# Optimization experiments

Hardware: AMD Instinct MI355X
Metric: run time of the kernel (lower is better)

The kernel has to match this reference:

```python
import jax, jax.numpy as jnp
from jax import lax
import numpy as np

C_IN = 64
C_OUT = 64
CQ = C_OUT // 8   # query/key channels
K = 5             # axial kernel length
RATIO = 0.7       # hybrid-norm mixing ratio
EPS = 1e-5
DN = ('NCHW', 'OIHW', 'NCHW')


def setup_inputs() -> dict:
    key = jax.random.key(0)
    ks = jax.random.split(key, 16)
    rn = lambda k, s, sc=0.05: jax.random.normal(k, s, dtype=jnp.float32) * sc
    return dict(
        x=jax.random.normal(ks[0], (4, C_IN, 256, 256), dtype=jnp.float32),
        hconv_w=rn(ks[1], (C_IN, 1, 1, K)), hconv_b=rn(ks[2], (C_IN,)),
        vconv_w=rn(ks[3], (C_IN, 1, K, 1)), vconv_b=rn(ks[4], (C_IN,)),
        pw_w=rn(ks[5], (C_OUT, C_IN)), pw_b=rn(ks[6], (C_OUT,)),
        bn_w=1.0 + rn(ks[7], (C_OUT,)), bn_b=rn(ks[8], (C_OUT,)),
        q_w=rn(ks[9], (CQ, C_OUT)), q_b=rn(ks[10], (CQ,)),
        k_w=rn(ks[11], (CQ, C_OUT)), k_b=rn(ks[12], (CQ,)),
        v_w=rn(ks[13], (C_OUT, C_OUT)), v_b=rn(ks[14], (C_OUT,)),
        gamma=rn(ks[15], (1,), 0.1),
    )


def reference(x, hconv_w, hconv_b, vconv_w, vconv_b, pw_w, pw_b,
              bn_w, bn_b, q_w, q_b, k_w, k_b, v_w, v_b, gamma):
    # ---- AxialDepthwiseConv: depthwise (1,K) + (K,1) + x, relu, pointwise ----
    h = lax.conv_general_dilated(x, hconv_w, (1, 1), [(0, 0), (K // 2, K // 2)],
                                 dimension_numbers=DN, feature_group_count=C_IN)
    h = h + hconv_b[:, None, None]
    v = lax.conv_general_dilated(x, vconv_w, (1, 1), [(K // 2, K // 2), (0, 0)],
                                 dimension_numbers=DN, feature_group_count=C_IN)
    v = v + vconv_b[:, None, None]
    a = jax.nn.relu(h + v + x)
    y = jnp.einsum('bchw,oc->bohw', a, pw_w) + pw_b[:, None, None]

    # ---- HybridNormalization: 0.7*InstanceNorm(no affine) + 0.3*BatchNorm(train) ----
    im = y.mean((2, 3), keepdims=True)
    iv = y.var((2, 3), keepdims=True)
    inn = (y - im) * lax.rsqrt(iv + EPS)
    bm = y.mean((0, 2, 3), keepdims=True)
    bv = y.var((0, 2, 3), keepdims=True)
    bnn = (y - bm) * lax.rsqrt(bv + EPS) * bn_w[:, None, None] + bn_b[:, None, None]
    y = RATIO * inn + (1.0 - RATIO) * bnn

    # ---- CrissCrossAttention ----
    q = jnp.einsum('bchw,oc->bohw', y, q_w) + q_b[:, None, None]   # (B,CQ,H,W)
    k = jnp.einsum('bchw,oc->bohw', y, k_w) + k_b[:, None, None]   # (B,CQ,H,W)
    val = jnp.einsum('bchw,oc->bohw', y, v_w) + v_b[:, None, None] # (B,C,H,W)

    # height (per column w): attn[b,w,j,i] = softmax_i( q[b,:,j,w] . k[b,:,i,w] )
    Ah = jax.nn.softmax(jnp.einsum('bcjw,bciw->bwji', q, k), axis=-1)
    # h_out[b,c,i,w] = sum_j val[b,c,j,w] * Ah[b,w,j,i]  (matches bmm(value, attn))
    h_out = jnp.einsum('bcjw,bwji->bciw', val, Ah)

    # width (per row h): attn[b,h,y,x] = softmax_x( q[b,:,h,y] . k[b,:,h,x] )
    Av = jax.nn.softmax(jnp.einsum('bchy,bchx->bhyx', q, k), axis=-1)
    v_out = jnp.einsum('bchy,bhyx->bchx', val, Av)

    out = gamma[0] * (h_out + v_out) + y

    # ---- MaxPool2d(2,2) ----
    down = lax.reduce_window(out, -jnp.inf, lax.max, (1, 1, 2, 2), (1, 1, 2, 2), 'VALID')
    return out, down
```

## Files before the change

kernel.cpp:

```cpp
#include <hip/hip_runtime.h>
#include <hip/hip_bf16.h>

#define Bn 4
#define Cc 64
#define CQn 8
#define Hh 256
#define Ww 256
#define PLANE 65536
#define LOG2E 1.4426950408889634f

typedef unsigned short ushortT;
typedef __attribute__((ext_vector_type(8))) unsigned short us8;
typedef __attribute__((ext_vector_type(4))) unsigned short us4;
typedef __attribute__((ext_vector_type(8))) __bf16 bf16x8;
typedef __attribute__((ext_vector_type(4))) float f32x4;

__device__ inline ushortT f2bf(float f) {
    __hip_bfloat16 h = __float2bfloat16(f);
    return *(ushortT*)&h;
}
__device__ inline float bf2f(ushortT u) {
    return __uint_as_float((unsigned)u << 16);
}
union BF8U { us8 u; bf16x8 b; uint4 w; };
__device__ inline us8 zero_us8() {
    BF8U z; z.w.x = 0; z.w.y = 0; z.w.z = 0; z.w.w = 0; return z.u;
}

__global__ void pack_weights_kernel(
    const float* __restrict__ pww, const float* __restrict__ qw,
    const float* __restrict__ kw, const float* __restrict__ vw,
    ushortT* __restrict__ pw_bf, ushortT* __restrict__ qk_bf,
    ushortT* __restrict__ vw_bf)
{
    int i = blockIdx.x * 256 + threadIdx.x;
    if (i < 64 * 64) pw_bf[i] = f2bf(pww[i]);
    if (i < 64 * 64) vw_bf[i] = f2bf(vw[i]);
    if (i < 8 * 64)  qk_bf[i] = f2bf(qw[i]);
    if (i >= 8 * 64 && i < 16 * 64) qk_bf[i] = f2bf(kw[i - 512]);
}

__global__ __launch_bounds__(256) void dw_kernel(
    const float* __restrict__ x,
    const float* __restrict__ hw, const float* __restrict__ hb,
    const float* __restrict__ vw, const float* __restrict__ vb,
    ushortT* __restrict__ aout)
{
    int blk = blockIdx.x;
    int bc = blk >> 4;
    int ht = blk & 15;
    int h0 = ht * 16;
    int c = bc & 63;
    int tid = threadIdx.x;
    __shared__ float rows[20][260];
    const float* xp = x + (size_t)bc * PLANE;
    #pragma unroll
    for (int i = 0; i < 20; ++i) {
        int hr = h0 - 2 + i;
        rows[i][tid + 2] = (hr >= 0 && hr < Hh) ? xp[hr * Ww + tid] : 0.f;
    }
    if (tid < 20) {
        rows[tid][0] = 0.f; rows[tid][1] = 0.f;
        rows[tid][258] = 0.f; rows[tid][259] = 0.f;
    }
    __syncthreads();

    float hw0 = hw[c * 5 + 0], hw1 = hw[c * 5 + 1], hw2 = hw[c * 5 + 2],
          hw3 = hw[c * 5 + 3], hw4 = hw[c * 5 + 4];
    float vw0 = vw[c * 5 + 0], vw1 = vw[c * 5 + 1], vw2 = vw[c * 5 + 2],
          vw3 = vw[c * 5 + 3], vw4 = vw[c * 5 + 4];
    float bias = hb[c] + vb[c];

    ushortT* op = aout + (size_t)bc * PLANE + h0 * Ww + tid;
    #pragma unroll
    for (int r = 0; r < 16; ++r) {
        float hs = hw0 * rows[r + 2][tid]     + hw1 * rows[r + 2][tid + 1]
                 + hw2 * rows[r + 2][tid + 2] + hw3 * rows[r + 2][tid + 3]
                 + hw4 * rows[r + 2][tid + 4];
        float vs = vw0 * rows[r][tid + 2]     + vw1 * rows[r + 1][tid + 2]
                 + vw2 * rows[r + 2][tid + 2] + vw3 * rows[r + 3][tid + 2]
                 + vw4 * rows[r + 4][tid + 2];
        float res = hs + vs + bias + rows[r + 2][tid + 2];
        op[r * Ww] = f2bf(fmaxf(res, 0.f));
    }
}

__global__ __launch_bounds__(256) void pw_mfma_kernel(
    const ushortT* __restrict__ a_bf, const ushortT* __restrict__ pw_bf,
    const float* __restrict__ pwb,
    float* __restrict__ y_raw, float* __restrict__ sums, float* __restrict__ sumsq)
{
    int blk = blockIdx.x;
    int b = blk >> 8;
    int t0 = (blk & 255) << 8;
    int tid = threadIdx.x, lane = tid & 63, wv = tid >> 6;
    int half = lane >> 4;
    int col = lane & 15;

    __shared__ ushortT ytile[256 * 74];

    {
        size_t base = (size_t)b * Cc * PLANE + t0 + tid;
        uint* wrow = (uint*)&ytile[tid * 74];
        #pragma unroll
        for (int c = 0; c < Cc; c += 2) {
            ushortT v0 = a_bf[base + (size_t)c * PLANE];
            ushortT v1 = a_bf[base + (size_t)(c + 1) * PLANE];
            wrow[c >> 1] = (uint)v0 | ((uint)v1 << 16);
        }
    }
    __syncthreads();

    int m0 = wv * 16;
    BF8U a0, a1;
    a0.u = *(const us8*)(pw_bf + (m0 + col) * 64 + half * 8);
    a1.u = *(const us8*)(pw_bf + (m0 + col) * 64 + 32 + half * 8);

    float bias[4], s[4], s2[4];
    #pragma unroll
    for (int r = 0; r < 4; ++r) {
        bias[r] = pwb[m0 + half * 4 + r];
        s[r] = 0.f; s2[r] = 0.f;
    }

    const uint* lw = (const uint*)ytile;
    #pragma unroll 4
    for (int t = 0; t < 16; ++t) {
        int rbase = (t * 16 + col) * 37 + half * 4;
        BF8U b0, b1;
        b0.w.x = lw[rbase];      b0.w.y = lw[rbase + 1];
        b0.w.z = lw[rbase + 2];  b0.w.w = lw[rbase + 3];
        b1.w.x = lw[rbase + 16]; b1.w.y = lw[rbase + 17];
        b1.w.z = lw[rbase + 18]; b1.w.w = lw[rbase + 19];
        f32x4 acc = (f32x4){0.f, 0.f, 0.f, 0.f};
        acc = __builtin_amdgcn_mfma_f32_16x16x32_bf16(a0.b, b0.b, acc, 0, 0, 0);
        acc = __builtin_amdgcn_mfma_f32_16x16x32_bf16(a1.b, b1.b, acc, 0, 0, 0);
        int pix = t * 16 + col;
        #pragma unroll
        for (int r = 0; r < 4; ++r) {
            int c = m0 + half * 4 + r;
            float v = acc[r] + bias[r];
            y_raw[(size_t)(b * Cc + c) * PLANE + t0 + pix] = v;
            s[r] += v; s2[r] += v * v;
        }
    }
    #pragma unroll
    for (int r = 0; r < 4; ++r) {
        #pragma unroll
        for (int d = 8; d > 0; d >>= 1) {
            s[r]  += __shfl_down(s[r], d, 16);
            s2[r] += __shfl_down(s2[r], d, 16);
        }
    }
    if (col == 0) {
        #pragma unroll
        for (int r = 0; r < 4; ++r) {
            int c = m0 + half * 4 + r;
            atomicAdd(&sums[b * Cc + c], s[r]);
            atomicAdd(&sumsq[b * Cc + c], s2[r]);
        }
    }
}

__global__ __launch_bounds__(256) void qkv_mfma_kernel(
    const float* __restrict__ y_raw,
    const float* __restrict__ sums, const float* __restrict__ sumsq,
    const float* __restrict__ bnw, const float* __restrict__ bnb,
    const ushortT* __restrict__ qk_bf, const float* __restrict__ qbias,
    const float* __restrict__ kbias,
    const ushortT* __restrict__ vw_bf, const float* __restrict__ vbias,
    ushortT* __restrict__ q, ushortT* __restrict__ k,
    ushortT* __restrict__ val)
{
    int blk = blockIdx.x;
    int b = blk >> 8;
    int t0 = (blk & 255) << 8;
    int tid = threadIdx.x, lane = tid & 63, wv = tid >> 6;
    int half = lane >> 4;
    int col = lane & 15;

    __shared__ ushortT ytile[256 * 74];
    __shared__ float alpha_s[64], beta_s[64];

    if (tid < 64) {
        int c = tid;
        float im[4], e2[4];
        float bm = 0.f, be2 = 0.f;
        #pragma unroll
        for (int bb = 0; bb < 4; ++bb) {
            im[bb] = sums[bb * Cc + c] * (1.f / 65536.f);
            e2[bb] = sumsq[bb * Cc + c] * (1.f / 65536.f);
            bm += im[bb]; be2 += e2[bb];
        }
        bm *= 0.25f; be2 *= 0.25f;
        float rsb = rsqrtf(be2 - bm * bm + 1e-5f);
        float wgt = bnw[c];
        float rsi = rsqrtf(e2[b] - im[b] * im[b] + 1e-5f);
        alpha_s[c] = 0.7f * rsi + 0.3f * rsb * wgt;
        beta_s[c]  = -0.7f * im[b] * rsi - 0.3f * bm * rsb * wgt + 0.3f * bnb[c];
    }
    __syncthreads();

    {
        size_t base = (size_t)b * Cc * PLANE + t0 + tid;
        uint* wrow = (uint*)&ytile[tid * 74];
        #pragma unroll
        for (int c = 0; c < Cc; c += 2) {
            float v0 = y_raw[base + (size_t)c * PLANE];
            float v1 = y_raw[base + (size_t)(c + 1) * PLANE];
            float n0 = alpha_s[c] * v0 + beta_s[c];
            float n1 = alpha_s[c + 1] * v1 + beta_s[c + 1];
            wrow[c >> 1] = (uint)f2bf(n0) | ((uint)f2bf(n1) << 16);
        }
    }
    __syncthreads();

    const uint* lw = (const uint*)ytile;

    {
        BF8U a0, a1;
        a0.u = *(const us8*)(qk_bf + col * 64 + half * 8);
        a1.u = *(const us8*)(qk_bf + col * 64 + 32 + half * 8);
        #pragma unroll
        for (int i = 0; i < 4; ++i) {
            int t = wv * 4 + i;
            int rbase = (t * 16 + col) * 37 + half * 4;
            BF8U b0, b1;
            b0.w.x = lw[rbase];      b0.w.y = lw[rbase + 1];
            b0.w.z = lw[rbase + 2];  b0.w.w = lw[rbase + 3];
            b1.w.x = lw[rbase + 16]; b1.w.y = lw[rbase + 17];
            b1.w.z = lw[rbase + 18]; b1.w.w = lw[rbase + 19];
            f32x4 acc = (f32x4){0.f, 0.f, 0.f, 0.f};
            acc = __builtin_amdgcn_mfma_f32_16x16x32_bf16(a0.b, b0.b, acc, 0, 0, 0);
            acc = __builtin_amdgcn_mfma_f32_16x16x32_bf16(a1.b, b1.b, acc, 0, 0, 0);
            int pix = t * 16 + col;
            #pragma unroll
            for (int r = 0; r < 4; ++r) {
                int row = half * 4 + r;
                if (row < 8)
                    q[(size_t)(b * CQn + row) * PLANE + t0 + pix] =
                        f2bf((acc[r] + qbias[row]) * LOG2E);
                else
                    k[(size_t)(b * CQn + row - 8) * PLANE + t0 + pix] = f2bf(acc[r] + kbias[row - 8]);
            }
        }
    }

    {
        int m0 = wv * 16;
        BF8U a0, a1;
        a0.u = *(const us8*)(vw_bf + (m0 + col) * 64 + half * 8);
        a1.u = *(const us8*)(vw_bf + (m0 + col) * 64 + 32 + half * 8);
        float bias[4];
        #pragma unroll
        for (int r = 0; r < 4; ++r) bias[r] = vbias[m0 + half * 4 + r];
        #pragma unroll 4
        for (int t = 0; t < 16; ++t) {
            int rbase = (t * 16 + col) * 37 + half * 4;
            BF8U b0, b1;
            b0.w.x = lw[rbase];      b0.w.y = lw[rbase + 1];
            b0.w.z = lw[rbase + 2];  b0.w.w = lw[rbase + 3];
            b1.w.x = lw[rbase + 16]; b1.w.y = lw[rbase + 17];
            b1.w.z = lw[rbase + 18]; b1.w.w = lw[rbase + 19];
            f32x4 acc = (f32x4){0.f, 0.f, 0.f, 0.f};
            acc = __builtin_amdgcn_mfma_f32_16x16x32_bf16(a0.b, b0.b, acc, 0, 0, 0);
            acc = __builtin_amdgcn_mfma_f32_16x16x32_bf16(a1.b, b1.b, acc, 0, 0, 0);
            int pix = t * 16 + col;
            #pragma unroll
            for (int r = 0; r < 4; ++r) {
                int c = m0 + half * 4 + r;
                val[(size_t)(b * Cc + c) * PLANE + t0 + pix] = f2bf(acc[r] + bias[r]);
            }
        }
    }
}

__global__ __launch_bounds__(256) void transpose_all_kernel(
    const ushortT* __restrict__ qb, ushortT* __restrict__ qT,
    const ushortT* __restrict__ kb, ushortT* __restrict__ kT,
    const ushortT* __restrict__ vb, ushortT* __restrict__ vT)
{
    int blk = blockIdx.x;
    int plane = blk >> 6;
    int tile = blk & 63;
    const ushortT* src; ushortT* dst;
    if (plane < 32)      { src = qb + (size_t)plane * PLANE;        dst = qT + (size_t)plane * PLANE; }
    else if (plane < 64) { src = kb + (size_t)(plane - 32) * PLANE; dst = kT + (size_t)(plane - 32) * PLANE; }
    else                 { src = vb + (size_t)(plane - 64) * PLANE; dst = vT + (size_t)(plane - 64) * PLANE; }
    int th = (tile >> 3) * 32;
    int tw = (tile & 7) * 32;
    __shared__ ushortT t[32][34];
    int lw = threadIdx.x & 31;
    int lh = threadIdx.x >> 5;
    #pragma unroll
    for (int i = 0; i < 4; ++i)
        t[lh + 8 * i][lw] = src[(th + lh + 8 * i) * Ww + tw + lw];
    __syncthreads();
    #pragma unroll
    for (int i = 0; i < 4; ++i)
        dst[(tw + lh + 8 * i) * Hh + th + lw] = t[lw][lh + 8 * i];
}

__global__ __launch_bounds__(256) void attn_kernel(
    const ushortT* __restrict__ q0, const ushortT* __restrict__ k0,
    const ushortT* __restrict__ v0, ushortT* __restrict__ o0,
    const ushortT* __restrict__ q1, const ushortT* __restrict__ k1,
    const ushortT* __restrict__ v1, ushortT* __restrict__ o1)
{
    int blk = blockIdx.x;
    int sel = blk >> 10;
    const ushortT* __restrict__ q   = sel ? q1 : q0;
    const ushortT* __restrict__ k   = sel ? k1 : k0;
    const ushortT* __restrict__ val = sel ? v1 : v0;
    ushortT* __restrict__ outp      = sel ? o1 : o0;
    int bblk = blk & 1023;
    int b = bblk >> 8;
    int r = bblk & 255;
    int tid = threadIdx.x;
    int lane = tid & 63;
    int wv = tid >> 6;
    int col = lane & 15;
    int quad = lane >> 4;

    __shared__ ushortT q_s[256 * 8];
    __shared__ ushortT k_s[256 * 8];
    __shared__ ushortT A_lds[2][4 * 256 * 8];
    __shared__ float mhat[256];
    __shared__ float kred[32];
    __shared__ float lsum[2][4][32];

    size_t vbase = (size_t)b * Cc * PLANE + (size_t)r * Ww
                 + (size_t)(wv * 16 + col) * PLANE + quad * 8;
    BF8U afb[2];
    afb[0].u = *(const us8*)(val + vbase);

    size_t qkbase = (size_t)b * CQn * PLANE + (size_t)r * Ww + tid;
    float qf[8], ka[8];
    {
        BF8U qp, kp;
        #pragma unroll
        for (int c = 0; c < 8; ++c) {
            ushortT qv = q[qkbase + (size_t)c * PLANE];
            ushortT kv = k[qkbase + (size_t)c * PLANE];
            qp.u[c] = qv; kp.u[c] = kv;
            qf[c] = bf2f(qv);
            ka[c] = fabsf(bf2f(kv));
        }
        *(us8*)&q_s[tid * 8] = qp.u;
        *(us8*)&k_s[tid * 8] = kp.u;
    }
    #pragma unroll
    for (int d = 1; d < 64; d <<= 1)
        #pragma unroll
        for (int c = 0; c < 8; ++c)
            ka[c] = fmaxf(ka[c], __shfl_xor(ka[c], d));
    if (lane == 0)
        #pragma unroll
        for (int c = 0; c < 8; ++c) kred[wv * 8 + c] = ka[c];
    __syncthreads();

    {
        float mh = 0.f;
        #pragma unroll
        for (int c = 0; c < 8; ++c) {
            float km = fmaxf(fmaxf(kred[c], kred[8 + c]),
                             fmaxf(kred[16 + c], kred[24 + c]));
            mh += fabsf(qf[c]) * km;
        }
        mhat[tid] = mh;
    }
    __syncthreads();

    BF8U kc[4];
    #pragma unroll
    for (int i = 0; i < 4; ++i)
        kc[i].u = *(const us8*)&k_s[((wv * 4 + i) * 16 + col) * 8];
    f32x4 acc[16];
    #pragma unroll
    for (int t = 0; t < 16; ++t) acc[t] = (f32x4){0.f, 0.f, 0.f, 0.f};

    auto compute_slab = [&](int kslab, int buf) {
        float ps[8];
        #pragma unroll
        for (int e = 0; e < 8; ++e) ps[e] = 0.f;
        #pragma unroll
        for (int jj2 = 0; jj2 < 2; ++jj2) {
            int jt = kslab * 2 + jj2;
            BF8U qa; qa.u = zero_us8();
            if (quad == 0) qa.u = *(const us8*)&q_s[(jt * 16 + col) * 8];
            float mh4[4];
            #pragma unroll
            for (int rr = 0; rr < 4; ++rr) mh4[rr] = mhat[jt * 16 + quad * 4 + rr];
            #pragma unroll
            for (int i = 0; i < 4; ++i) {
                f32x4 sacc = (f32x4){0.f, 0.f, 0.f, 0.f};
                sacc = __builtin_amdgcn_mfma_f32_16x16x32_bf16(qa.b, kc[i].b, sacc, 0, 0, 0);
                us4 pk;
                #pragma unroll
                for (int rr = 0; rr < 4; ++rr) {
                    float e = __builtin_amdgcn_exp2f(sacc[rr] - mh4[rr]);
                    ps[jj2 * 4 + rr] += e;
                    pk[rr] = f2bf(e);
                }
                int irow = (wv * 4 + i) * 16 + col;
                int jq = jj2 * 2 + (quad >> 1);
                *(us4*)&A_lds[buf][(jq * 256 + irow) * 8 + (quad & 1) * 4] = pk;
            }
        }
        #pragma unroll
        for (int d = 1; d < 16; d <<= 1)
            #pragma unroll
            for (int e = 0; e < 8; ++e)
                ps[e] += __shfl_xor(ps[e], d);
        if (col == 0) {
            #pragma unroll
            for (int jj2 = 0; jj2 < 2; ++jj2)
                #pragma unroll
                for (int rr = 0; rr < 4; ++rr)
                    lsum[buf][wv][jj2 * 16 + quad * 4 + rr] = ps[jj2 * 4 + rr];
        }
    };

    compute_slab(0, 0);
    __syncthreads();

    #pragma unroll
    for (int ks = 0; ks < 8; ++ks) {
        int cur = ks & 1;
        if (ks < 7) {
            afb[cur ^ 1].u = *(const us8*)(val + vbase + (ks + 1) * 32);
            compute_slab(ks + 1, cur ^ 1);
        }
        f32x4 l0 = *(const f32x4*)&lsum[cur][0][quad * 8];
        f32x4 l1 = *(const f32x4*)&lsum[cur][0][quad * 8 + 4];
        #pragma unroll
        for (int w = 1; w < 4; ++w) {
            l0 += *(const f32x4*)&lsum[cur][w][quad * 8];
            l1 += *(const f32x4*)&lsum[cur][w][quad * 8 + 4];
        }
        BF8U av;
        #pragma unroll
        for (int e = 0; e < 4; ++e) {
            av.u[e]     = f2bf(bf2f(afb[cur].u[e])     * __builtin_amdgcn_rcpf(l0[e]));
            av.u[4 + e] = f2bf(bf2f(afb[cur].u[4 + e]) * __builtin_amdgcn_rcpf(l1[e]));
        }
        #pragma unroll
        for (int t = 0; t < 16; ++t) {
            BF8U bfr;
            bfr.u = *(const us8*)&A_lds[cur][(quad * 256 + t * 16 + col) * 8];
            acc[t] = __builtin_amdgcn_mfma_f32_16x16x32_bf16(av.b, bfr.b, acc[t], 0, 0, 0);
        }
        __syncthreads();
    }

    size_t obase = (size_t)b * Cc * PLANE + (size_t)r * Ww;
    #pragma unroll
    for (int t = 0; t < 16; ++t) {
        int i = t * 16 + col;
        #pragma unroll
        for (int rr = 0; rr < 4; ++rr) {
            int c = wv * 16 + quad * 4 + rr;
            outp[obase + (size_t)c * PLANE + i] = f2bf(acc[t][rr]);
        }
    }
}

__global__ __launch_bounds__(256) void final_kernel(
    const ushortT* __restrict__ houtT, const ushortT* __restrict__ hout0,
    const float* __restrict__ y_raw,
    const float* __restrict__ sums, const float* __restrict__ sumsq,
    const float* __restrict__ bnw, const float* __restrict__ bnb,
    const float* __restrict__ gamma,
    float* __restrict__ out, float* __restrict__ down)
{
    int blk = blockIdx.x;
    int tile = blk & 63;
    int bc = blk >> 6;
    int b = bc >> 6;
    int c = bc & 63;
    int th = (tile >> 3) * 32;
    int tw = (tile & 7) * 32;

    float im[4], e2[4];
    float bm = 0.f, be2 = 0.f;
    #pragma unroll
    for (int bb = 0; bb < 4; ++bb) {
        im[bb] = sums[bb * Cc + c] * (1.f / 65536.f);
        e2[bb] = sumsq[bb * Cc + c] * (1.f / 65536.f);
        bm += im[bb]; be2 += e2[bb];
    }
    bm *= 0.25f; be2 *= 0.25f;
    float rsb = rsqrtf(be2 - bm * bm + 1e-5f);
    float wgt = bnw[c];
    float rsi = rsqrtf(e2[b] - im[b] * im[b] + 1e-5f);
    float al = 0.7f * rsi + 0.3f * rsb * wgt;
    float bt = -0.7f * im[b] * rsi - 0.3f * bm * rsb * wgt + 0.3f * bnb[c];

    __shared__ float t[32][33];
    const ushortT* hT = houtT + (size_t)bc * PLANE;
    {
        int ww = threadIdx.x >> 3;
        int hh = (threadIdx.x & 7) * 4;
        us4 v4 = *(const us4*)(hT + (size_t)(tw + ww) * Hh + th + hh);
        t[hh + 0][ww] = __uint_as_float((unsigned)v4[0] << 16);
        t[hh + 1][ww] = __uint_as_float((unsigned)v4[1] << 16);
        t[hh + 2][ww] = __uint_as_float((unsigned)v4[2] << 16);
        t[hh + 3][ww] = __uint_as_float((unsigned)v4[3] << 16);
    }
    __syncthreads();
    float g = gamma[0];
    int qw_ = threadIdx.x & 15;
    int qh_ = threadIdx.x >> 4;
    const float* yb = y_raw + (size_t)bc * PLANE;
    const ushortT* hb = hout0 + (size_t)bc * PLANE;
    float* ob = out + (size_t)bc * PLANE;
    float mx = -1e30f;
    float2 res[2];
    #pragma unroll
    for (int i = 0; i < 2; ++i) {
        int hh = 2 * qh_ + i;
        int off = (th + hh) * Ww + tw + 2 * qw_;
        uint hv = *(const uint*)(hb + off);
        float2 y = *(const float2*)(yb + off);
        float y0 = al * y.x + bt;
        float y1 = al * y.y + bt;
        float o0 = g * (t[hh][2 * qw_]     + bf2f((ushortT)(hv & 0xffff))) + y0;
        float o1 = g * (t[hh][2 * qw_ + 1] + bf2f((ushortT)(hv >> 16)))   + y1;
        res[i] = make_float2(o0, o1);
        mx = fmaxf(mx, fmaxf(o0, o1));
    }
    #pragma unroll
    for (int i = 0; i < 2; ++i) {
        int off = (th + 2 * qh_ + i) * Ww + tw + 2 * qw_;
        *(float2*)(ob + off) = res[i];
    }
    down[(size_t)bc * 16384 + (th / 2 + qh_) * 128 + tw / 2 + qw_] = mx;
}

extern "C" void kernel_launch(void* const* d_in, const int* in_sizes, int n_in,
                              void* d_out, int out_size, void* d_ws, size_t ws_size,
                              hipStream_t stream)
{
    const float* x     = (const float*)d_in[0];
    const float* hw    = (const float*)d_in[1];
    const float* hb    = (const float*)d_in[2];
    const float* vw    = (const float*)d_in[3];
    const float* vb    = (const float*)d_in[4];
    const float* pww   = (const float*)d_in[5];
    const float* pwb   = (const float*)d_in[6];
    const float* bnw   = (const float*)d_in[7];
    const float* bnb   = (const float*)d_in[8];
    const float* qw    = (const float*)d_in[9];
    const float* qb    = (const float*)d_in[10];
    const float* kw    = (const float*)d_in[11];
    const float* kb    = (const float*)d_in[12];
    const float* vw2   = (const float*)d_in[13];
    const float* vb2   = (const float*)d_in[14];
    const float* gamma = (const float*)d_in[15];

    float* ws = (float*)d_ws;
    const size_t NP = (size_t)Bn * Cc * PLANE;
    const size_t NQ = (size_t)Bn * CQn * PLANE;
    float* y_raw  = ws;
    float* slotB  = ws + NP;
    float* slotC  = ws + 2 * NP;
    float* slotD  = ws + 2 * NP + NP / 2;
    float* ptr    = ws + 3 * NP;
    ushortT* qbuf = (ushortT*)ptr;
    ushortT* kbuf = qbuf + NQ;
    ushortT* qT   = kbuf + NQ;
    ushortT* kT   = qT + NQ;
    float* sums   = (float*)(kT + NQ);
    float* sumsq  = sums + 256;
    ushortT* pw_bf = (ushortT*)(sumsq + 256);
    ushortT* qk_bf = pw_bf + 64 * 64;
    ushortT* vw_bf = qk_bf + 16 * 64;

    ushortT* a_buf = (ushortT*)slotC;
    ushortT* valT  = (ushortT*)slotC;
    ushortT* valb  = (ushortT*)slotD;
    ushortT* hout0 = (ushortT*)slotB;
    ushortT* houtT = hout0 + NP;
    float* out  = (float*)d_out;
    float* down = out + NP;

    hipMemsetAsync(sums, 0, 512 * sizeof(float), stream);
    pack_weights_kernel<<<dim3(16), dim3(256), 0, stream>>>(
        pww, qw, kw, vw2, pw_bf, qk_bf, vw_bf);
    dw_kernel<<<dim3(Bn * Cc * 16), dim3(256), 0, stream>>>(
        x, hw, hb, vw, vb, a_buf);
    pw_mfma_kernel<<<dim3(Bn * 256), dim3(256), 0, stream>>>(
        a_buf, pw_bf, pwb, y_raw, sums, sumsq);
    qkv_mfma_kernel<<<dim3(Bn * 256), dim3(256), 0, stream>>>(
        y_raw, sums, sumsq, bnw, bnb, qk_bf, qb, kb, vw_bf, vb2,
        qbuf, kbuf, valb);
    transpose_all_kernel<<<dim3(320 * 64), dim3(256), 0, stream>>>(
        qbuf, qT, kbuf, kT, valb, valT);
    attn_kernel<<<dim3(2 * Bn * Hh), dim3(256), 0, stream>>>(
        qbuf, kbuf, valb, hout0, qT, kT, valT, houtT);
    final_kernel<<<dim3(Bn * Cc * 64), dim3(256), 0, stream>>>(
        houtT, hout0, y_raw, sums, sumsq, bnw, bnb, gamma, out, down);
}
```

Baseline: 369.8 us.

## Precompute log-sum-exp row shift in separate pass, fold softmax normalization into exponent

Adds a first pass that computes each query row's softmax denominator and stores the shift (max bound plus log of the sum) in shared memory. The main loop then exponentiates directly with that shift, so probabilities come out already normalized. This removes the per-slab partial sums, their cross-wave reduction, and the rescaling of the value fragment by reciprocals. The cost is computing every QK score and exponential twice, adding MFMA and transcendental work plus a log and an extra barrier.

```diff
diff --git a/kernel.cpp b/kernel.cpp
--- a/kernel.cpp
+++ b/kernel.cpp
@@ -326,8 +326,8 @@
     __shared__ ushortT k_s[256 * 8];
     __shared__ ushortT A_lds[2][4 * 256 * 8];
     __shared__ float mhat[256];
+    __shared__ float shiftv[256];
     __shared__ float kred[32];
-    __shared__ float lsum[2][4][32];
 
     size_t vbase = (size_t)b * Cc * PLANE + (size_t)r * Ww
                  + (size_t)(wv * 16 + col) * PLANE + quad * 8;
@@ -371,6 +371,36 @@
     }
     __syncthreads();
 
+    #pragma unroll
+    for (int t = 0; t < 4; ++t) {
+        int jt = wv * 4 + t;
+        BF8U qa; qa.u = zero_us8();
+        if (quad == 0) qa.u = *(const us8*)&q_s[(jt * 16 + col) * 8];
+        float mh4[4];
+        #pragma unroll
+        for (int rr = 0; rr < 4; ++rr) mh4[rr] = mhat[jt * 16 + quad * 4 + rr];
+        f32x4 ls = (f32x4){0.f, 0.f, 0.f, 0.f};
+        for (int it = 0; it < 16; ++it) {
+            BF8U kb;
+            kb.u = *(const us8*)&k_s[(it * 16 + col) * 8];
+            f32x4 sacc = (f32x4){0.f, 0.f, 0.f, 0.f};
+            sacc = __builtin_amdgcn_mfma_f32_16x16x32_bf16(qa.b, kb.b, sacc, 0, 0, 0);
+            #pragma unroll
+            for (int rr = 0; rr < 4; ++rr)
+                ls[rr] += __builtin_amdgcn_exp2f(sacc[rr] - mh4[rr]);
+        }
+        #pragma unroll
+        for (int d = 1; d < 16; d <<= 1)
+            #pragma unroll
+            for (int rr = 0; rr < 4; ++rr)
+                ls[rr] += __shfl_xor(ls[rr], d);
+        if (col == 0)
+            #pragma unroll
+            for (int rr = 0; rr < 4; ++rr)
+                shiftv[jt * 16 + quad * 4 + rr] = mh4[rr] + __builtin_amdgcn_logf(ls[rr]);
+    }
+    __syncthreads();
+
     BF8U kc[4];
     #pragma unroll
     for (int i = 0; i < 4; ++i)
@@ -379,49 +409,31 @@
     #pragma unroll
     for (int t = 0; t < 16; ++t) acc[t] = (f32x4){0.f, 0.f, 0.f, 0.f};
 
-    auto compute_slab = [&](int kslab, int buf) {
-        float ps[8];
-        #pragma unroll
-        for (int e = 0; e < 8; ++e) ps[e] = 0.f;
+    auto compute_E = [&](int kslab, int buf) {
         #pragma unroll
         for (int jj2 = 0; jj2 < 2; ++jj2) {
             int jt = kslab * 2 + jj2;
             BF8U qa; qa.u = zero_us8();
             if (quad == 0) qa.u = *(const us8*)&q_s[(jt * 16 + col) * 8];
-            float mh4[4];
+            float sh4[4];
             #pragma unroll
-            for (int rr = 0; rr < 4; ++rr) mh4[rr] = mhat[jt * 16 + quad * 4 + rr];
+            for (int rr = 0; rr < 4; ++rr) sh4[rr] = shiftv[jt * 16 + quad * 4 + rr];
             #pragma unroll
             for (int i = 0; i < 4; ++i) {
                 f32x4 sacc = (f32x4){0.f, 0.f, 0.f, 0.f};
                 sacc = __builtin_amdgcn_mfma_f32_16x16x32_bf16(qa.b, kc[i].b, sacc, 0, 0, 0);
                 us4 pk;
                 #pragma unroll
-                for (int rr = 0; rr < 4; ++rr) {
-                    float e = __builtin_amdgcn_exp2f(sacc[rr] - mh4[rr]);
-                    ps[jj2 * 4 + rr] += e;
-                    pk[rr] = f2bf(e);
-                }
+                for (int rr = 0; rr < 4; ++rr)
+                    pk[rr] = f2bf(__builtin_amdgcn_exp2f(sacc[rr] - sh4[rr]));
                 int irow = (wv * 4 + i) * 16 + col;
                 int jq = jj2 * 2 + (quad >> 1);
                 *(us4*)&A_lds[buf][(jq * 256 + irow) * 8 + (quad & 1) * 4] = pk;
             }
         }
-        #pragma unroll
-        for (int d = 1; d < 16; d <<= 1)
-            #pragma unroll
-            for (int e = 0; e < 8; ++e)
-                ps[e] += __shfl_xor(ps[e], d);
-        if (col == 0) {
-            #pragma unroll
-            for (int jj2 = 0; jj2 < 2; ++jj2)
-                #pragma unroll
-                for (int rr = 0; rr < 4; ++rr)
-                    lsum[buf][wv][jj2 * 16 + quad * 4 + rr] = ps[jj2 * 4 + rr];
-        }
     };
 
-    compute_slab(0, 0);
+    compute_E(0, 0);
     __syncthreads();
 
     #pragma unroll
@@ -429,26 +441,13 @@
         int cur = ks & 1;
         if (ks < 7) {
             afb[cur ^ 1].u = *(const us8*)(val + vbase + (ks + 1) * 32);
-            compute_slab(ks + 1, cur ^ 1);
-        }
-        f32x4 l0 = *(const f32x4*)&lsum[cur][0][quad * 8];
-        f32x4 l1 = *(const f32x4*)&lsum[cur][0][quad * 8 + 4];
-        #pragma unroll
-        for (int w = 1; w < 4; ++w) {
-            l0 += *(const f32x4*)&lsum[cur][w][quad * 8];
-            l1 += *(const f32x4*)&lsum[cur][w][quad * 8 + 4];
-        }
-        BF8U av;
-        #pragma unroll
-        for (int e = 0; e < 4; ++e) {
-            av.u[e]     = f2bf(bf2f(afb[cur].u[e])     * __builtin_amdgcn_rcpf(l0[e]));
-            av.u[4 + e] = f2bf(bf2f(afb[cur].u[4 + e]) * __builtin_amdgcn_rcpf(l1[e]));
+            compute_E(ks + 1, cur ^ 1);
         }
         #pragma unroll
         for (int t = 0; t < 16; ++t) {
             BF8U bfr;
             bfr.u = *(const us8*)&A_lds[cur][(quad * 256 + t * 16 + col) * 8];
-            acc[t] = __builtin_amdgcn_mfma_f32_16x16x32_bf16(av.b, bfr.b, acc[t], 0, 0, 0);
+            acc[t] = __builtin_amdgcn_mfma_f32_16x16x32_bf16(afb[cur].b, bfr.b, acc[t], 0, 0, 0);
         }
         __syncthreads();
     }
```

Result: no change. 364.3 us (-1.5%).
